# Kernel tuning notes

Hardware: AMD Instinct MI355X
Metric: run time of the kernel (lower is better)

Reference implementation:

```python
import jax, jax.numpy as jnp
import numpy as np

B, T, C = 2, 2048, 2048
N_HEADS, N_KV_HEADS = 16, 4
HEAD_DIM = C // N_HEADS  # 128
NUM_GROUPS = N_HEADS // N_KV_HEADS  # 4


def setup_inputs() -> dict:
    key = jax.random.key(0)
    ks = jax.random.split(key, 5)
    s = 1.0 / np.sqrt(C)
    return {
        "x": jax.random.normal(ks[0], (B, T, C), dtype=jnp.float32),
        "Wq": jax.random.normal(ks[1], (C, N_HEADS * HEAD_DIM), dtype=jnp.float32) * s,
        "Wk": jax.random.normal(ks[2], (C, N_KV_HEADS * HEAD_DIM), dtype=jnp.float32) * s,
        "Wv": jax.random.normal(ks[3], (C, N_KV_HEADS * HEAD_DIM), dtype=jnp.float32) * s,
        "Wo": jax.random.normal(ks[4], (C, C), dtype=jnp.float32) * s,
    }


def _rope_tables(seq_len, head_dim, dtype):
    theta = 1.0 / (10000.0 ** (jnp.arange(0, head_dim, 2, dtype=jnp.float32) / head_dim))
    freqs = jnp.arange(seq_len, dtype=jnp.float32)[:, None] * theta[None, :]  # [T, hd/2]
    cos = jnp.concatenate([jnp.cos(freqs), jnp.cos(freqs)], axis=-1)  # [T, hd]
    sin = jnp.concatenate([jnp.sin(freqs), jnp.sin(freqs)], axis=-1)
    return cos.astype(dtype), sin.astype(dtype)


def _rotate_half(x):
    x1, x2 = jnp.split(x, 2, axis=-1)
    return jnp.concatenate([-x2, x1], axis=-1)


def reference(x, Wq, Wk, Wv, Wo):
    b, t, c = x.shape
    q = (x @ Wq).reshape(b, t, N_HEADS, HEAD_DIM).transpose(0, 2, 1, 3)      # [B,H,T,hd]
    k = (x @ Wk).reshape(b, t, N_KV_HEADS, HEAD_DIM).transpose(0, 2, 1, 3)   # [B,Hkv,T,hd]
    v = (x @ Wv).reshape(b, t, N_KV_HEADS, HEAD_DIM).transpose(0, 2, 1, 3)

    cos, sin = _rope_tables(t, HEAD_DIM, x.dtype)  # [T,hd]
    cos = cos[None, None]  # [1,1,T,hd]
    sin = sin[None, None]
    q = q * cos + _rotate_half(q) * sin
    k = k * cos + _rotate_half(k) * sin

    # GQA: expand kv heads (repeat_interleave along head dim)
    k = jnp.repeat(k, NUM_GROUPS, axis=1)  # [B,H,T,hd]
    v = jnp.repeat(v, NUM_GROUPS, axis=1)

    scale = 1.0 / jnp.sqrt(jnp.asarray(HEAD_DIM, dtype=x.dtype))
    scores = jnp.einsum("bhqd,bhkd->bhqk", q, k) * scale  # [B,H,T,T]
    causal = jnp.tril(jnp.ones((t, t), dtype=bool))
    scores = jnp.where(causal[None, None], scores, jnp.asarray(-jnp.inf, dtype=scores.dtype))
    attn = jax.nn.softmax(scores, axis=-1)
    out = jnp.einsum("bhqk,bhkd->bhqd", attn, v)  # [B,H,T,hd]
    out = out.transpose(0, 2, 1, 3).reshape(b, t, c)
    return out @ Wo
```

## Files before the change

### kernel.cpp

```cpp
#include <hip/hip_runtime.h>
#include <hip/hip_bf16.h>
#include <math.h>

typedef __hip_bfloat16 bf16;
typedef __attribute__((ext_vector_type(8))) short bf16x8;
typedef __attribute__((ext_vector_type(4))) float floatx4;

__device__ __forceinline__ void async_copy16(const bf16* g, bf16* l) {
    __builtin_amdgcn_global_load_lds(
        (__attribute__((address_space(1))) void*)(void*)g,
        (__attribute__((address_space(3))) void*)(void*)l,
        16, 0, 0);
}

__global__ __launch_bounds__(256) void cast_f32_bf16(const float* __restrict__ in,
                                                     bf16* __restrict__ out, int n4) {
    int i = blockIdx.x * 256 + threadIdx.x;
    if (i >= n4) return;
    float4 v = ((const float4*)in)[i];
    union { ushort4 u; bf16 b[4]; } o;
    o.b[0] = __float2bfloat16(v.x);
    o.b[1] = __float2bfloat16(v.y);
    o.b[2] = __float2bfloat16(v.z);
    o.b[3] = __float2bfloat16(v.w);
    ((ushort4*)out)[i] = o.u;
}

__global__ __launch_bounds__(256) void cast_transpose(const float* __restrict__ in,
                                                      bf16* __restrict__ out, int K, int N) {
    __shared__ float tile[32][33];
    int nb = blockIdx.x * 32, kb = blockIdx.y * 32;
    for (int j = threadIdx.y; j < 32; j += 8)
        tile[j][threadIdx.x] = in[(size_t)(kb + j) * N + nb + threadIdx.x];
    __syncthreads();
    for (int j = threadIdx.y; j < 32; j += 8)
        out[(size_t)(nb + j) * K + kb + threadIdx.x] = __float2bfloat16(tile[threadIdx.x][j]);
}

template <bool OUTF32>
__global__ __launch_bounds__(256) void gemm_bt(const bf16* __restrict__ A,
                                               const bf16* __restrict__ Bt,
                                               void* __restrict__ Cout,
                                               int M, int N, int K) {
    __shared__ bf16 As[128 * 32];
    __shared__ bf16 Bs[128 * 32];
    const int tid = threadIdx.x;
    const int wave = tid >> 6, lane = tid & 63;
    const int c = lane & 15, quad = lane >> 4;
    const int wm = wave >> 1, wn = wave & 1;
    const int mBase = blockIdx.y * 128, nBase = blockIdx.x * 128;

    const int sRow = lane >> 2;
    const int sCol = (lane & 3) << 3;
    const bf16* gA = A + (size_t)(mBase + wave * 32 + sRow) * K + sCol;
    const bf16* gB = Bt + (size_t)(nBase + wave * 32 + sRow) * K + sCol;
    bf16* lA = As + wave * 1024;
    bf16* lB = Bs + wave * 1024;

    floatx4 acc[4][4];
#pragma unroll
    for (int mt = 0; mt < 4; mt++)
#pragma unroll
        for (int nt = 0; nt < 4; nt++) acc[mt][nt] = (floatx4){0.f, 0.f, 0.f, 0.f};

    for (int k0 = 0; k0 < K; k0 += 32) {
        async_copy16(gA + k0, lA);
        async_copy16(gA + k0 + 16 * K, lA + 512);
        async_copy16(gB + k0, lB);
        async_copy16(gB + k0 + 16 * K, lB + 512);
        __syncthreads();
        bf16x8 af[4], bfr[4];
#pragma unroll
        for (int mt = 0; mt < 4; mt++)
            af[mt] = *(const bf16x8*)(As + (wm * 64 + mt * 16 + c) * 32 + quad * 8);
#pragma unroll
        for (int nt = 0; nt < 4; nt++)
            bfr[nt] = *(const bf16x8*)(Bs + (wn * 64 + nt * 16 + c) * 32 + quad * 8);
#pragma unroll
        for (int mt = 0; mt < 4; mt++)
#pragma unroll
            for (int nt = 0; nt < 4; nt++)
                acc[mt][nt] = __builtin_amdgcn_mfma_f32_16x16x32_bf16(af[mt], bfr[nt],
                                                                      acc[mt][nt], 0, 0, 0);
        __syncthreads();
    }
#pragma unroll
    for (int mt = 0; mt < 4; mt++)
#pragma unroll
        for (int nt = 0; nt < 4; nt++)
#pragma unroll
            for (int r = 0; r < 4; r++) {
                int row = mBase + wm * 64 + mt * 16 + quad * 4 + r;
                int col = nBase + wn * 64 + nt * 16 + c;
                if (OUTF32)
                    ((float*)Cout)[(size_t)row * N + col] = acc[mt][nt][r];
                else
                    ((bf16*)Cout)[(size_t)row * N + col] = __float2bfloat16(acc[mt][nt][r]);
            }
}

__global__ __launch_bounds__(256) void rope_kernel(bf16* __restrict__ X, int heads, int rowStride) {
    int idx = blockIdx.x * 256 + threadIdx.x;
    int d = idx & 63;
    int h = (idx >> 6) % heads;
    int row = idx / (heads * 64);
    int t = row & 2047;
    float theta = exp2f(-(float)d * 0.20762050593045827f);
    float ang = (float)t * theta;
    float sv, cv;
    __sincosf(ang, &sv, &cv);
    bf16* p = X + (size_t)row * rowStride + h * 128 + d;
    float x1 = __bfloat162float(p[0]);
    float x2 = __bfloat162float(p[64]);
    p[0]  = __float2bfloat16(x1 * cv - x2 * sv);
    p[64] = __float2bfloat16(x2 * cv + x1 * sv);
}

__global__ __launch_bounds__(256) void vtrans(const bf16* __restrict__ QKV,
                                              bf16* __restrict__ Vtg) {
    __shared__ bf16 tile[32][34];
    const int bh = blockIdx.z;
    const int b = bh >> 2, kvh = bh & 3;
    const int t0 = blockIdx.x * 32, d0 = blockIdx.y * 32;
    const bf16* src = QKV + (size_t)b * 2048 * 3072 + 2560 + kvh * 128;
    for (int j = threadIdx.y; j < 32; j += 8)
        tile[j][threadIdx.x] = src[(size_t)(t0 + j) * 3072 + d0 + threadIdx.x];
    __syncthreads();
    bf16* dst = Vtg + (size_t)bh * 128 * 2048;
    for (int j = threadIdx.y; j < 32; j += 8)
        dst[(size_t)(d0 + j) * 2048 + t0 + threadIdx.x] = tile[threadIdx.x][j];
}

__global__ __launch_bounds__(256, 2) void flash_attn2(const bf16* __restrict__ QKV,
                                                      const bf16* __restrict__ Vtg,
                                                      bf16* __restrict__ AO) {
    const int T = 2048, STR = 3072;
    __shared__ bf16 Ks[4 * 64 * 32];
    __shared__ bf16 Vs[2 * 128 * 32];
    __shared__ bf16 Pl[4][2][16 * 40];
    const int b = blockIdx.z, h = blockIdx.y, pj = blockIdx.x;
    const int kvh = h >> 2;
    const int tid = threadIdx.x, wave = tid >> 6, lane = tid & 63;
    const int c = lane & 15, quad = lane >> 4;
    const float C2 = 0.12751541717525597f;

    const bf16* Kg = QKV + (size_t)b * T * STR + 2048 + kvh * 128;
    const bf16* Vg = Vtg + (size_t)(b * 4 + kvh) * 128 * 2048;
    const int srow = tid >> 2;
    const int scol = (tid & 3) * 8;
    bf16* PlW = &Pl[wave][0][0];

    for (int phase = 0; phase < 2; phase++) {
        const int q0 = ((phase == 0) ? pj : (31 - pj)) * 64;
        bf16x8 qf[4];
        {
            const bf16* qp = QKV + ((size_t)b * T + q0 + wave * 16 + c) * STR + h * 128 + quad * 8;
#pragma unroll
            for (int ks = 0; ks < 4; ks++) qf[ks] = *(const bf16x8*)(qp + ks * 32);
        }
        floatx4 accO[8];
#pragma unroll
        for (int nt = 0; nt < 8; nt++) accO[nt] = (floatx4){0.f, 0.f, 0.f, 0.f};
        float lrow[4] = {0.f, 0.f, 0.f, 0.f};

        for (int kt0 = 0; kt0 <= q0; kt0 += 64) {
            const bool diag = (kt0 == q0);
#pragma unroll
            for (int it = 0; it < 4; it++) {
                async_copy16(Kg + (size_t)(kt0 + srow) * STR + it * 32 + scol,
                             Ks + it * 2048 + wave * 512);
                async_copy16(Vg + (size_t)((it & 1) * 64 + srow) * 2048 + kt0 + (it >> 1) * 32 + scol,
                             Vs + it * 2048 + wave * 512);
            }
            __syncthreads();
            floatx4 sf[4];
#pragma unroll
            for (int nt = 0; nt < 4; nt++) sf[nt] = (floatx4){0.f, 0.f, 0.f, 0.f};
#pragma unroll
            for (int ks = 0; ks < 4; ks++)
#pragma unroll
                for (int nt = 0; nt < 4; nt++) {
                    bf16x8 kf = *(const bf16x8*)(Ks + ks * 2048 + (nt * 16 + c) * 32 + quad * 8);
                    sf[nt] = __builtin_amdgcn_mfma_f32_16x16x32_bf16(qf[ks], kf, sf[nt], 0, 0, 0);
                }
#pragma unroll
            for (int nt = 0; nt < 4; nt++)
#pragma unroll
                for (int r = 0; r < 4; r++) {
                    float p = exp2f(sf[nt][r] * C2);
                    int lim = diag ? (wave * 16 + quad * 4 + r) : 63;
                    if (nt * 16 + c > lim) p = 0.f;
                    lrow[r] += p;
                    PlW[(nt >> 1) * 640 + (quad * 4 + r) * 40 + (nt & 1) * 16 + c] =
                        __float2bfloat16(p);
                }
#pragma unroll
            for (int kc = 0; kc < 2; kc++) {
                bf16x8 pf = *(const bf16x8*)(PlW + kc * 640 + c * 40 + quad * 8);
#pragma unroll
                for (int nt = 0; nt < 8; nt++) {
                    bf16x8 vf = *(const bf16x8*)(Vs + kc * 4096 + (nt * 16 + c) * 32 + quad * 8);
                    accO[nt] = __builtin_amdgcn_mfma_f32_16x16x32_bf16(pf, vf, accO[nt], 0, 0, 0);
                }
            }
            __syncthreads();
        }
        float inv[4];
#pragma unroll
        for (int r = 0; r < 4; r++) {
            float s = lrow[r];
            s += __shfl_xor(s, 1);
            s += __shfl_xor(s, 2);
            s += __shfl_xor(s, 4);
            s += __shfl_xor(s, 8);
            inv[r] = 1.0f / s;
        }
        const size_t orow = (size_t)b * T + q0 + wave * 16 + quad * 4;
#pragma unroll
        for (int nt = 0; nt < 8; nt++)
#pragma unroll
            for (int r = 0; r < 4; r++)
                AO[(orow + r) * 2048 + h * 128 + nt * 16 + c] =
                    __float2bfloat16(accO[nt][r] * inv[r]);
    }
}

extern "C" void kernel_launch(void* const* d_in, const int* in_sizes, int n_in,
                              void* d_out, int out_size, void* d_ws, size_t ws_size,
                              hipStream_t stream) {
    const float* x  = (const float*)d_in[0];
    const float* Wq = (const float*)d_in[1];
    const float* Wk = (const float*)d_in[2];
    const float* Wv = (const float*)d_in[3];
    const float* Wo = (const float*)d_in[4];

    char* ws = (char*)d_ws;
    bf16* xb  = (bf16*)(ws);
    bf16* Vtg = (bf16*)(ws);
    bf16* Wt  = (bf16*)(ws + 16777216);
    bf16* Wot = (bf16*)(ws + 29360128);
    bf16* QKV = (bf16*)(ws + 37748736);
    bf16* AO  = (bf16*)(ws + 62914560);

    cast_f32_bf16<<<8192, 256, 0, stream>>>(x, xb, 2097152);
    cast_transpose<<<dim3(64, 64), dim3(32, 8), 0, stream>>>(Wq, Wt, 2048, 2048);
    cast_transpose<<<dim3(16, 64), dim3(32, 8), 0, stream>>>(Wk, Wt + 2048 * 2048, 2048, 512);
    cast_transpose<<<dim3(16, 64), dim3(32, 8), 0, stream>>>(Wv, Wt + 2560 * 2048, 2048, 512);
    cast_transpose<<<dim3(64, 64), dim3(32, 8), 0, stream>>>(Wo, Wot, 2048, 2048);

    gemm_bt<false><<<dim3(24, 32), 256, 0, stream>>>(xb, Wt, QKV, 4096, 3072, 2048);

    rope_kernel<<<16384, 256, 0, stream>>>(QKV, 16, 3072);
    rope_kernel<<<4096, 256, 0, stream>>>(QKV + 2048, 4, 3072);

    vtrans<<<dim3(64, 4, 8), dim3(32, 8), 0, stream>>>(QKV, Vtg);

    flash_attn2<<<dim3(16, 16, 2), 256, 0, stream>>>(QKV, Vtg, AO);

    gemm_bt<true><<<dim3(16, 32), 256, 0, stream>>>(AO, Wot, d_out, 4096, 2048, 2048);
}
```

Before: 336.3 us.

## Fuse Q RoPE into attention, swizzle LDS, one q-tile per block

Adds an XOR swizzle to the LDS tile layout in both the GEMM and attention kernels to cut bank conflicts. Q RoPE is now computed in registers inside the attention kernel, so the separate Q rope pass over global memory goes away. The attention grid becomes one 64-row q-tile per block, launched longest-first, instead of pairing two tiles per block. Occupancy is raised to 4 blocks per CU, the P buffer is halved, and the diagonal mask is specialised at compile time. The catch: Q RoPE is recomputed with sincos per block, and the added register pressure may cause spills.

```diff
diff --git a/kernel.cpp b/kernel.cpp
--- a/kernel.cpp
+++ b/kernel.cpp
@@ -1,6 +1,7 @@
 #include <hip/hip_runtime.h>
 #include <hip/hip_bf16.h>
 #include <math.h>
+#include <utility>
 
 typedef __hip_bfloat16 bf16;
 typedef __attribute__((ext_vector_type(8))) short bf16x8;
@@ -51,7 +52,8 @@
     const int mBase = blockIdx.y * 128, nBase = blockIdx.x * 128;
 
     const int sRow = lane >> 2;
-    const int sCol = (lane & 3) << 3;
+    const int sCol = ((lane & 3) ^ ((lane >> 3) & 3)) << 3;
+    const int rdOff = (quad ^ ((c >> 1) & 3)) << 3;
     const bf16* gA = A + (size_t)(mBase + wave * 32 + sRow) * K + sCol;
     const bf16* gB = Bt + (size_t)(nBase + wave * 32 + sRow) * K + sCol;
     bf16* lA = As + wave * 1024;
@@ -72,10 +74,10 @@
         bf16x8 af[4], bfr[4];
 #pragma unroll
         for (int mt = 0; mt < 4; mt++)
-            af[mt] = *(const bf16x8*)(As + (wm * 64 + mt * 16 + c) * 32 + quad * 8);
+            af[mt] = *(const bf16x8*)(As + (wm * 64 + mt * 16 + c) * 32 + rdOff);
 #pragma unroll
         for (int nt = 0; nt < 4; nt++)
-            bfr[nt] = *(const bf16x8*)(Bs + (wn * 64 + nt * 16 + c) * 32 + quad * 8);
+            bfr[nt] = *(const bf16x8*)(Bs + (wn * 64 + nt * 16 + c) * 32 + rdOff);
 #pragma unroll
         for (int mt = 0; mt < 4; mt++)
 #pragma unroll
@@ -131,14 +133,16 @@
         dst[(size_t)(d0 + j) * 2048 + t0 + threadIdx.x] = tile[threadIdx.x][j];
 }
 
-__global__ __launch_bounds__(256, 2) void flash_attn2(const bf16* __restrict__ QKV,
+__global__ __launch_bounds__(256, 4) void flash_attn3(const bf16* __restrict__ QKV,
                                                       const bf16* __restrict__ Vtg,
                                                       bf16* __restrict__ AO) {
     const int T = 2048, STR = 3072;
     __shared__ bf16 Ks[4 * 64 * 32];
     __shared__ bf16 Vs[2 * 128 * 32];
-    __shared__ bf16 Pl[4][2][16 * 40];
-    const int b = blockIdx.z, h = blockIdx.y, pj = blockIdx.x;
+    __shared__ bf16 Pl[4][16 * 40];
+    const int b = blockIdx.z, h = blockIdx.y;
+    const int qtile = 31 - blockIdx.x;
+    const int q0 = qtile * 64;
     const int kvh = h >> 2;
     const int tid = threadIdx.x, wave = tid >> 6, lane = tid & 63;
     const int c = lane & 15, quad = lane >> 4;
@@ -147,82 +151,103 @@
     const bf16* Kg = QKV + (size_t)b * T * STR + 2048 + kvh * 128;
     const bf16* Vg = Vtg + (size_t)(b * 4 + kvh) * 128 * 2048;
     const int srow = tid >> 2;
-    const int scol = (tid & 3) * 8;
-    bf16* PlW = &Pl[wave][0][0];
-
-    for (int phase = 0; phase < 2; phase++) {
-        const int q0 = ((phase == 0) ? pj : (31 - pj)) * 64;
-        bf16x8 qf[4];
-        {
-            const bf16* qp = QKV + ((size_t)b * T + q0 + wave * 16 + c) * STR + h * 128 + quad * 8;
-#pragma unroll
-            for (int ks = 0; ks < 4; ks++) qf[ks] = *(const bf16x8*)(qp + ks * 32);
+    const int xcol = ((tid & 3) ^ ((tid >> 3) & 3)) << 3;
+    const int koff = (quad ^ ((c >> 1) & 3)) << 3;
+    bf16* PlW = &Pl[wave][0];
+
+    bf16x8 qf[4];
+    {
+        const bf16* qp = QKV + ((size_t)b * T + q0 + wave * 16 + c) * STR + h * 128 + quad * 8;
+#pragma unroll
+        for (int ks = 0; ks < 4; ks++) qf[ks] = *(const bf16x8*)(qp + ks * 32);
+        const float t = (float)(q0 + wave * 16 + c);
+#pragma unroll
+        for (int ks = 0; ks < 2; ks++)
+#pragma unroll
+            for (int j = 0; j < 8; j++) {
+                int d = ks * 32 + quad * 8 + j;
+                float theta = exp2f((float)d * -0.20762050593045827f);
+                float sv, cv;
+                __sincosf(t * theta, &sv, &cv);
+                float lo = __bfloat162float(((const bf16*)&qf[ks])[j]);
+                float hi = __bfloat162float(((const bf16*)&qf[ks + 2])[j]);
+                ((bf16*)&qf[ks])[j]     = __float2bfloat16(lo * cv - hi * sv);
+                ((bf16*)&qf[ks + 2])[j] = __float2bfloat16(hi * cv + lo * sv);
+            }
+    }
+
+    floatx4 accO[8];
+#pragma unroll
+    for (int nt = 0; nt < 8; nt++) accO[nt] = (floatx4){0.f, 0.f, 0.f, 0.f};
+    float lrow[4] = {0.f, 0.f, 0.f, 0.f};
+
+    auto tile = [&](int kt0, auto DIAGC) {
+        constexpr bool DIAG = decltype(DIAGC)::value;
+#pragma unroll
+        for (int it = 0; it < 4; it++) {
+            async_copy16(Kg + (size_t)(kt0 + srow) * STR + it * 32 + xcol,
+                         Ks + it * 2048 + wave * 512);
+            async_copy16(Vg + (size_t)((it & 1) * 64 + srow) * 2048 + kt0 + (it >> 1) * 32 + xcol,
+                         Vs + it * 2048 + wave * 512);
         }
-        floatx4 accO[8];
-#pragma unroll
-        for (int nt = 0; nt < 8; nt++) accO[nt] = (floatx4){0.f, 0.f, 0.f, 0.f};
-        float lrow[4] = {0.f, 0.f, 0.f, 0.f};
-
-        for (int kt0 = 0; kt0 <= q0; kt0 += 64) {
-            const bool diag = (kt0 == q0);
-#pragma unroll
-            for (int it = 0; it < 4; it++) {
-                async_copy16(Kg + (size_t)(kt0 + srow) * STR + it * 32 + scol,
-                             Ks + it * 2048 + wave * 512);
-                async_copy16(Vg + (size_t)((it & 1) * 64 + srow) * 2048 + kt0 + (it >> 1) * 32 + scol,
-                             Vs + it * 2048 + wave * 512);
-            }
-            __syncthreads();
-            floatx4 sf[4];
-#pragma unroll
-            for (int nt = 0; nt < 4; nt++) sf[nt] = (floatx4){0.f, 0.f, 0.f, 0.f};
-#pragma unroll
-            for (int ks = 0; ks < 4; ks++)
-#pragma unroll
-                for (int nt = 0; nt < 4; nt++) {
-                    bf16x8 kf = *(const bf16x8*)(Ks + ks * 2048 + (nt * 16 + c) * 32 + quad * 8);
-                    sf[nt] = __builtin_amdgcn_mfma_f32_16x16x32_bf16(qf[ks], kf, sf[nt], 0, 0, 0);
-                }
-#pragma unroll
-            for (int nt = 0; nt < 4; nt++)
+        __syncthreads();
+        floatx4 sf[4];
+#pragma unroll
+        for (int nt = 0; nt < 4; nt++) sf[nt] = (floatx4){0.f, 0.f, 0.f, 0.f};
+#pragma unroll
+        for (int ks = 0; ks < 4; ks++)
+#pragma unroll
+            for (int nt = 0; nt < 4; nt++) {
+                bf16x8 kf = *(const bf16x8*)(Ks + ks * 2048 + (nt * 16 + c) * 32 + koff);
+                sf[nt] = __builtin_amdgcn_mfma_f32_16x16x32_bf16(qf[ks], kf, sf[nt], 0, 0, 0);
+            }
+#pragma unroll
+        for (int kc = 0; kc < 2; kc++) {
+#pragma unroll
+            for (int nt2 = 0; nt2 < 2; nt2++) {
+                const int nt = kc * 2 + nt2;
 #pragma unroll
                 for (int r = 0; r < 4; r++) {
                     float p = exp2f(sf[nt][r] * C2);
-                    int lim = diag ? (wave * 16 + quad * 4 + r) : 63;
-                    if (nt * 16 + c > lim) p = 0.f;
+                    if (DIAG)
+                        if (nt * 16 + c > wave * 16 + quad * 4 + r) p = 0.f;
                     lrow[r] += p;
-                    PlW[(nt >> 1) * 640 + (quad * 4 + r) * 40 + (nt & 1) * 16 + c] =
-                        __float2bfloat16(p);
+                    PlW[(quad * 4 + r) * 40 + nt2 * 16 + c] = __float2bfloat16(p);
                 }
-#pragma unroll
-            for (int kc = 0; kc < 2; kc++) {
-                bf16x8 pf = *(const bf16x8*)(PlW + kc * 640 + c * 40 + quad * 8);
-#pragma unroll
-                for (int nt = 0; nt < 8; nt++) {
-                    bf16x8 vf = *(const bf16x8*)(Vs + kc * 4096 + (nt * 16 + c) * 32 + quad * 8);
-                    accO[nt] = __builtin_amdgcn_mfma_f32_16x16x32_bf16(pf, vf, accO[nt], 0, 0, 0);
-                }
-            }
-            __syncthreads();
+            }
+            asm volatile("s_waitcnt lgkmcnt(0)" ::: "memory");
+            bf16x8 pf = *(const bf16x8*)(PlW + c * 40 + quad * 8);
+#pragma unroll
+            for (int nt = 0; nt < 8; nt++) {
+                bf16x8 vf = *(const bf16x8*)(Vs + kc * 4096 + (nt * 16 + c) * 32 + koff);
+                accO[nt] = __builtin_amdgcn_mfma_f32_16x16x32_bf16(pf, vf, accO[nt], 0, 0, 0);
+            }
+            asm volatile("" ::: "memory");
         }
-        float inv[4];
-#pragma unroll
-        for (int r = 0; r < 4; r++) {
-            float s = lrow[r];
-            s += __shfl_xor(s, 1);
-            s += __shfl_xor(s, 2);
-            s += __shfl_xor(s, 4);
-            s += __shfl_xor(s, 8);
-            inv[r] = 1.0f / s;
-        }
-        const size_t orow = (size_t)b * T + q0 + wave * 16 + quad * 4;
-#pragma unroll
-        for (int nt = 0; nt < 8; nt++)
-#pragma unroll
-            for (int r = 0; r < 4; r++)
-                AO[(orow + r) * 2048 + h * 128 + nt * 16 + c] =
-                    __float2bfloat16(accO[nt][r] * inv[r]);
+        __syncthreads();
+    };
+
+    for (int kt0 = 0; kt0 < q0; kt0 += 64)
+        tile(kt0, std::integral_constant<bool, false>{});
+    tile(q0, std::integral_constant<bool, true>{});
+
+    float inv[4];
+#pragma unroll
+    for (int r = 0; r < 4; r++) {
+        float s = lrow[r];
+        s += __shfl_xor(s, 1);
+        s += __shfl_xor(s, 2);
+        s += __shfl_xor(s, 4);
+        s += __shfl_xor(s, 8);
+        inv[r] = 1.0f / s;
     }
+    const size_t orow = (size_t)b * T + q0 + wave * 16 + quad * 4;
+#pragma unroll
+    for (int nt = 0; nt < 8; nt++)
+#pragma unroll
+        for (int r = 0; r < 4; r++)
+            AO[(orow + r) * 2048 + h * 128 + nt * 16 + c] =
+                __float2bfloat16(accO[nt][r] * inv[r]);
 }
 
 extern "C" void kernel_launch(void* const* d_in, const int* in_sizes, int n_in,
@@ -250,12 +275,11 @@
 
     gemm_bt<false><<<dim3(24, 32), 256, 0, stream>>>(xb, Wt, QKV, 4096, 3072, 2048);
 
-    rope_kernel<<<16384, 256, 0, stream>>>(QKV, 16, 3072);
     rope_kernel<<<4096, 256, 0, stream>>>(QKV + 2048, 4, 3072);
 
     vtrans<<<dim3(64, 4, 8), dim3(32, 8), 0, stream>>>(QKV, Vtg);
 
-    flash_attn2<<<dim3(16, 16, 2), 256, 0, stream>>>(QKV, Vtg, AO);
+    flash_attn3<<<dim3(32, 16, 2), 256, 0, stream>>>(QKV, Vtg, AO);
 
     gemm_bt<true><<<dim3(16, 32), 256, 0, stream>>>(AO, Wot, d_out, 4096, 2048, 2048);
 }
```

Result: slower. 359.6 us (+6.9%).
